# Kernel tuning notes

Hardware: AMD Instinct MI355X
Metric: run time of the kernel (lower is better)

## Reference

```python
import jax, jax.numpy as jnp
import numpy as np

D = 1024
DFF = 4096  # SwiGLU hidden = 4*d_model
EPS = 1e-6

def rmsnorm(x, w):
    return x * jax.lax.rsqrt(jnp.mean(x * x, axis=-1, keepdims=True) + EPS) * w

def mingru_scan(gates, cands):
    # h_t = g_t * h_{t-1} + (1 - g_t) * c_t, h_0 = 0 -> linear recurrence,
    # solved with an associative scan over pairs (a, b): h = a*h_prev + b.
    a = gates
    b = (1.0 - gates) * cands
    def combine(e1, e2):
        a1, b1 = e1
        a2, b2 = e2
        return (a1 * a2, a2 * b1 + b2)
    _, h = jax.lax.associative_scan(combine, (a, b), axis=1)
    return h

def setup_inputs() -> dict:
    key = jax.random.key(0)
    ks = jax.random.split(key, 10)
    xavier = lambda k, fan_in, fan_out: jax.random.uniform(
        k, (fan_in, fan_out), jnp.float32,
        -np.sqrt(6.0 / (fan_in + fan_out)), np.sqrt(6.0 / (fan_in + fan_out)))
    return {
        "x": jax.random.normal(ks[0], (4, 4096, D), jnp.float32),
        "Wg": xavier(ks[1], D, D),
        "bg": jnp.ones((D,), jnp.float32),   # gate bias init = 1.0
        "Wc": xavier(ks[2], D, D),
        "bc": jnp.zeros((D,), jnp.float32),
        "n1_w": jnp.ones((D,), jnp.float32),
        "n2_w": jnp.ones((D,), jnp.float32),
        "W1": xavier(ks[3], D, DFF),   # SwiGLU gate proj
        "W3": xavier(ks[4], D, DFF),   # SwiGLU up proj
        "W2": xavier(ks[5], DFF, D),   # SwiGLU down proj
    }

def reference(x, Wg, bg, Wc, bc, n1_w, n2_w, W1, W3, W2):
    # --- MinGRU sub-block (pre-norm, residual) ---
    h_in = rmsnorm(x, n1_w)
    gates = jax.nn.sigmoid(jnp.einsum('bld,de->ble', h_in, Wg) + bg)
    cands = jnp.tanh(jnp.einsum('bld,de->ble', h_in, Wc) + bc)
    x = x + mingru_scan(gates, cands)
    # --- SwiGLU FFN sub-block (pre-norm, residual) ---
    f_in = rmsnorm(x, n2_w)
    ff = jnp.einsum('blf,fd->bld',
                    jax.nn.silu(jnp.einsum('bld,df->blf', f_in, W1))
                    * jnp.einsum('bld,df->blf', f_in, W3), W2)
    return x + ff
```

## Files before the change

kernel.cpp:

```cpp
#include <hip/hip_runtime.h>
#include <hip/hip_bf16.h>
#include <math.h>

typedef __bf16 bf16_t;
typedef bf16_t bf16x8 __attribute__((ext_vector_type(8)));
typedef bf16_t bf16x4 __attribute__((ext_vector_type(4)));
typedef bf16_t bf16x2 __attribute__((ext_vector_type(2)));
typedef float f32x4 __attribute__((ext_vector_type(4)));

#define D_MODEL 1024
#define SEQ     4096
#define BATCH   4
#define NTOK    16384
#define DFF     4096
#define CLEN    64
#define NCHUNK  64
#define NCH     4096

__device__ __forceinline__ void gload16(const bf16_t* g, bf16_t* l) {
    __builtin_amdgcn_global_load_lds(
        (const __attribute__((address_space(1))) void*)g,
        (__attribute__((address_space(3))) void*)l, 16, 0, 0);
}

__global__ void transpose_to_bf16(const float* __restrict__ W,
                                  bf16_t* __restrict__ Wt, int R, int C) {
    __shared__ float tile[32][33];
    const int c0 = blockIdx.x * 32, r0 = blockIdx.y * 32;
    const int tx = threadIdx.x, ty = threadIdx.y;
#pragma unroll
    for (int j = 0; j < 32; j += 8)
        tile[ty + j][tx] = W[(size_t)(r0 + ty + j) * C + c0 + tx];
    __syncthreads();
#pragma unroll
    for (int j = 0; j < 32; j += 8)
        Wt[(size_t)(c0 + ty + j) * R + r0 + tx] = (bf16_t)tile[tx][ty + j];
}

__global__ void rmsnorm_kernel(const float* __restrict__ x,
                               const float* __restrict__ w,
                               bf16_t* __restrict__ out) {
    const int row = blockIdx.x;
    const int tid = threadIdx.x;
    const float4 v = ((const float4*)(x + (size_t)row * D_MODEL))[tid];
    float ss = v.x * v.x + v.y * v.y + v.z * v.z + v.w * v.w;
#pragma unroll
    for (int o = 1; o < 64; o <<= 1) ss += __shfl_xor(ss, o);
    __shared__ float red[4];
    if ((tid & 63) == 0) red[tid >> 6] = ss;
    __syncthreads();
    const float tot = red[0] + red[1] + red[2] + red[3];
    const float scale = rsqrtf(tot * (1.0f / D_MODEL) + 1e-6f);
    const float4 wv = ((const float4*)w)[tid];
    bf16x4 o4;
    o4[0] = (bf16_t)(v.x * scale * wv.x);
    o4[1] = (bf16_t)(v.y * scale * wv.y);
    o4[2] = (bf16_t)(v.z * scale * wv.z);
    o4[3] = (bf16_t)(v.w * scale * wv.w);
    ((bf16x4*)(out + (size_t)row * D_MODEL))[tid] = o4;
}

template <int MODE>
__global__ __launch_bounds__(256, 2)
void gemm_dual(const bf16_t* __restrict__ A, const bf16_t* __restrict__ B1t,
               const bf16_t* __restrict__ B2t, const float* __restrict__ bias1,
               const float* __restrict__ bias2, bf16x2* __restrict__ GC,
               bf16_t* __restrict__ Ot, int N, int K) {
    __shared__ bf16_t As[128 * 32];
    __shared__ bf16_t B1s[128 * 32];
    __shared__ bf16_t B2s[128 * 32];
    const int tid = threadIdx.x;
    const int lane = tid & 63;
    const int wave = tid >> 6;
    const int bn = blockIdx.x, bm = blockIdx.y;

    const int stR = wave * 16 + (lane >> 2);
    const int stC = (lane & 3) * 8;
    const bf16_t* Ag  = A   + (size_t)(bm * 128 + stR) * K + stC;
    const bf16_t* B1g = B1t + (size_t)(bn * 128 + stR) * K + stC;
    const bf16_t* B2g = B2t + (size_t)(bn * 128 + stR) * K + stC;
    bf16_t* Al0  = &As [(wave * 16) * 32];
    bf16_t* Al1  = &As [(64 + wave * 16) * 32];
    bf16_t* B1l0 = &B1s[(wave * 16) * 32];
    bf16_t* B1l1 = &B1s[(64 + wave * 16) * 32];
    bf16_t* B2l0 = &B2s[(wave * 16) * 32];
    bf16_t* B2l1 = &B2s[(64 + wave * 16) * 32];
    const size_t row64 = (size_t)64 * K;

    const int wr = wave >> 1, wc = wave & 1;
    const int lr = lane & 15, lk = lane >> 4;

    f32x4 acc1[4][4] = {};
    f32x4 acc2[4][4] = {};
    for (int k0 = 0; k0 < K; k0 += 32) {
        __syncthreads();
        gload16(Ag  + k0,         Al0);
        gload16(Ag  + k0 + row64, Al1);
        gload16(B1g + k0,         B1l0);
        gload16(B1g + k0 + row64, B1l1);
        gload16(B2g + k0,         B2l0);
        gload16(B2g + k0 + row64, B2l1);
        __syncthreads();
        bf16x8 af[4], b1f[4], b2f[4];
#pragma unroll
        for (int m = 0; m < 4; ++m)
            af[m] = *(const bf16x8*)&As[(wr * 64 + m * 16 + lr) * 32 + lk * 8];
#pragma unroll
        for (int n = 0; n < 4; ++n) {
            b1f[n] = *(const bf16x8*)&B1s[(wc * 64 + n * 16 + lr) * 32 + lk * 8];
            b2f[n] = *(const bf16x8*)&B2s[(wc * 64 + n * 16 + lr) * 32 + lk * 8];
        }
#pragma unroll
        for (int m = 0; m < 4; ++m)
#pragma unroll
            for (int n = 0; n < 4; ++n) {
                acc1[m][n] = __builtin_amdgcn_mfma_f32_16x16x32_bf16(
                    af[m], b1f[n], acc1[m][n], 0, 0, 0);
                acc2[m][n] = __builtin_amdgcn_mfma_f32_16x16x32_bf16(
                    af[m], b2f[n], acc2[m][n], 0, 0, 0);
            }
    }
    const int rowBase = bm * 128 + wr * 64;
    const int colBase = bn * 128 + wc * 64;
#pragma unroll
    for (int n = 0; n < 4; ++n) {
        const int col = colBase + n * 16 + lr;
        float b1v = 0.f, b2v = 0.f;
        if (MODE == 0) { b1v = bias1[col]; b2v = bias2[col]; }
#pragma unroll
        for (int m = 0; m < 4; ++m) {
#pragma unroll
            for (int j = 0; j < 4; ++j) {
                const int row = rowBase + m * 16 + lk * 4 + j;
                const size_t idx = (size_t)row * N + col;
                if (MODE == 0) {
                    const float gv = 1.0f / (1.0f + __expf(-(acc1[m][n][j] + b1v)));
                    const float cv = tanhf(acc2[m][n][j] + b2v);
                    bf16x2 pk;
                    pk[0] = (bf16_t)gv;
                    pk[1] = (bf16_t)cv;
                    GC[idx] = pk;
                } else {
                    const float a = acc1[m][n][j];
                    const float s = a / (1.0f + __expf(-a));
                    Ot[idx] = (bf16_t)(s * acc2[m][n][j]);
                }
            }
        }
    }
}

__global__ __launch_bounds__(256, 2)
void gemm_res(const bf16_t* __restrict__ A, const bf16_t* __restrict__ Bt,
              float* O, int N, int K) {
    __shared__ bf16_t As[128 * 32];
    __shared__ bf16_t Bs[128 * 32];
    const int tid = threadIdx.x;
    const int lane = tid & 63;
    const int wave = tid >> 6;
    const int bn = blockIdx.x, bm = blockIdx.y;

    const int stR = wave * 16 + (lane >> 2);
    const int stC = (lane & 3) * 8;
    const bf16_t* Ag = A  + (size_t)(bm * 128 + stR) * K + stC;
    const bf16_t* Bg = Bt + (size_t)(bn * 128 + stR) * K + stC;
    bf16_t* Al0 = &As[(wave * 16) * 32];
    bf16_t* Al1 = &As[(64 + wave * 16) * 32];
    bf16_t* Bl0 = &Bs[(wave * 16) * 32];
    bf16_t* Bl1 = &Bs[(64 + wave * 16) * 32];
    const size_t row64 = (size_t)64 * K;

    const int wr = wave >> 1, wc = wave & 1;
    const int lr = lane & 15, lk = lane >> 4;

    f32x4 acc[4][4] = {};
    for (int k0 = 0; k0 < K; k0 += 32) {
        __syncthreads();
        gload16(Ag + k0,         Al0);
        gload16(Ag + k0 + row64, Al1);
        gload16(Bg + k0,         Bl0);
        gload16(Bg + k0 + row64, Bl1);
        __syncthreads();
        bf16x8 af[4], bf[4];
#pragma unroll
        for (int m = 0; m < 4; ++m)
            af[m] = *(const bf16x8*)&As[(wr * 64 + m * 16 + lr) * 32 + lk * 8];
#pragma unroll
        for (int n = 0; n < 4; ++n)
            bf[n] = *(const bf16x8*)&Bs[(wc * 64 + n * 16 + lr) * 32 + lk * 8];
#pragma unroll
        for (int m = 0; m < 4; ++m)
#pragma unroll
            for (int n = 0; n < 4; ++n)
                acc[m][n] = __builtin_amdgcn_mfma_f32_16x16x32_bf16(
                    af[m], bf[n], acc[m][n], 0, 0, 0);
    }
    const int rowBase = bm * 128 + wr * 64;
    const int colBase = bn * 128 + wc * 64;
#pragma unroll
    for (int n = 0; n < 4; ++n) {
        const int col = colBase + n * 16 + lr;
#pragma unroll
        for (int m = 0; m < 4; ++m) {
#pragma unroll
            for (int j = 0; j < 4; ++j) {
                const int row = rowBase + m * 16 + lk * 4 + j;
                const size_t idx = (size_t)row * N + col;
                O[idx] += acc[m][n][j];
            }
        }
    }
}

__global__ void scan_phase1(const bf16x2* __restrict__ gc,
                            float* __restrict__ cA, float* __restrict__ cB) {
    const int d = blockIdx.x * 256 + threadIdx.x;
    const int b = blockIdx.y;
    const int cidx = blockIdx.z;
    const int ch = b * D_MODEL + d;
    const size_t base = ((size_t)b * SEQ + (size_t)cidx * CLEN) * D_MODEL + d;
    float A = 1.0f, Bv = 0.0f;
#pragma unroll 8
    for (int t = 0; t < CLEN; ++t) {
        const bf16x2 v = gc[base + (size_t)t * D_MODEL];
        const float gv = (float)v[0], cv = (float)v[1];
        Bv = gv * Bv + (1.0f - gv) * cv;
        A *= gv;
    }
    cA[cidx * NCH + ch] = A;
    cB[cidx * NCH + ch] = Bv;
}

__global__ void scan_phase2(const float* __restrict__ cA,
                            const float* __restrict__ cB,
                            float* __restrict__ hstart) {
    const int ch = blockIdx.x * 256 + threadIdx.x;
    float h = 0.0f;
#pragma unroll 8
    for (int cdx = 0; cdx < NCHUNK; ++cdx) {
        hstart[cdx * NCH + ch] = h;
        h = cA[cdx * NCH + ch] * h + cB[cdx * NCH + ch];
    }
}

__global__ void scan_phase3(const bf16x2* __restrict__ gc,
                            const float* __restrict__ hstart,
                            const float* __restrict__ x,
                            float* __restrict__ x1) {
    const int d = blockIdx.x * 256 + threadIdx.x;
    const int b = blockIdx.y;
    const int cidx = blockIdx.z;
    const int ch = b * D_MODEL + d;
    const size_t base = ((size_t)b * SEQ + (size_t)cidx * CLEN) * D_MODEL + d;
    float h = hstart[cidx * NCH + ch];
#pragma unroll 8
    for (int t = 0; t < CLEN; ++t) {
        const size_t off = base + (size_t)t * D_MODEL;
        const bf16x2 v = gc[off];
        const float gv = (float)v[0], cv = (float)v[1];
        h = gv * h + (1.0f - gv) * cv;
        x1[off] = x[off] + h;
    }
}

extern "C" void kernel_launch(void* const* d_in, const int* in_sizes, int n_in,
                              void* d_out, int out_size, void* d_ws,
                              size_t ws_size, hipStream_t stream) {
    const float* x   = (const float*)d_in[0];
    const float* Wg  = (const float*)d_in[1];
    const float* bg  = (const float*)d_in[2];
    const float* Wc  = (const float*)d_in[3];
    const float* bc  = (const float*)d_in[4];
    const float* n1w = (const float*)d_in[5];
    const float* n2w = (const float*)d_in[6];
    const float* W1  = (const float*)d_in[7];
    const float* W3  = (const float*)d_in[8];
    const float* W2  = (const float*)d_in[9];
    float* out = (float*)d_out;

    char* p = (char*)d_ws;
    bf16_t* tbuf  = (bf16_t*)p;
    bf16_t* h_in  = (bf16_t*)p;  p += (size_t)NTOK * D_MODEL * 2;
    bf16x2* gcbuf = (bf16x2*)p;  p += (size_t)NTOK * D_MODEL * 4;
    p += (size_t)32 << 20;
    bf16_t* f_in  = (bf16_t*)p;  p += (size_t)NTOK * D_MODEL * 2;
    bf16_t* Wg_t  = (bf16_t*)p;  p += (size_t)D_MODEL * D_MODEL * 2;
    bf16_t* Wc_t  = (bf16_t*)p;  p += (size_t)D_MODEL * D_MODEL * 2;
    bf16_t* W1_t  = (bf16_t*)p;  p += (size_t)DFF * D_MODEL * 2;
    bf16_t* W3_t  = (bf16_t*)p;  p += (size_t)DFF * D_MODEL * 2;
    bf16_t* W2_t  = (bf16_t*)p;  p += (size_t)D_MODEL * DFF * 2;
    float* cA     = (float*)p;   p += (size_t)NCHUNK * NCH * 4;
    float* cB     = (float*)p;   p += (size_t)NCHUNK * NCH * 4;
    float* hstart = (float*)p;   p += (size_t)NCHUNK * NCH * 4;

    const dim3 tb(32, 8);
    transpose_to_bf16<<<dim3(1024 / 32, 1024 / 32), tb, 0, stream>>>(Wg, Wg_t, 1024, 1024);
    transpose_to_bf16<<<dim3(1024 / 32, 1024 / 32), tb, 0, stream>>>(Wc, Wc_t, 1024, 1024);
    transpose_to_bf16<<<dim3(4096 / 32, 1024 / 32), tb, 0, stream>>>(W1, W1_t, 1024, 4096);
    transpose_to_bf16<<<dim3(4096 / 32, 1024 / 32), tb, 0, stream>>>(W3, W3_t, 1024, 4096);
    transpose_to_bf16<<<dim3(1024 / 32, 4096 / 32), tb, 0, stream>>>(W2, W2_t, 4096, 1024);

    rmsnorm_kernel<<<NTOK, 256, 0, stream>>>(x, n1w, h_in);

    gemm_dual<0><<<dim3(D_MODEL / 128, NTOK / 128), 256, 0, stream>>>(
        h_in, Wg_t, Wc_t, bg, bc, gcbuf, nullptr, D_MODEL, D_MODEL);

    scan_phase1<<<dim3(D_MODEL / 256, BATCH, NCHUNK), 256, 0, stream>>>(gcbuf, cA, cB);
    scan_phase2<<<NCH / 256, 256, 0, stream>>>(cA, cB, hstart);
    scan_phase3<<<dim3(D_MODEL / 256, BATCH, NCHUNK), 256, 0, stream>>>(gcbuf, hstart, x, out);

    rmsnorm_kernel<<<NTOK, 256, 0, stream>>>(out, n2w, f_in);

    gemm_dual<1><<<dim3(DFF / 128, NTOK / 128), 256, 0, stream>>>(
        f_in, W1_t, W3_t, nullptr, nullptr, nullptr, tbuf, DFF, D_MODEL);

    gemm_res<<<dim3(D_MODEL / 128, NTOK / 128), 256, 0, stream>>>(tbuf, W2_t, out, D_MODEL, DFF);
}
```

Before: 847.9 us.

## Replace GEMMs with 8-wave double-buffered 256-row tiles, swizzled LDS and ping-pong schedule

Replaces the three GEMM kernels with one templated 512-thread kernel. It uses 256-row tiles, a K-step of 64 and double-buffered LDS staging of the next tile during compute. LDS rows are XOR-swizzled, which targets bank conflicts. Work-group ids are remapped in groups of 8 for cache locality, and barriers plus setprio stagger the MFMA and load phases. The aim is to hide global-load latency and raise MFMA utilisation, at the cost of much larger LDS use (128KB), high register pressure and reduced occupancy.

```diff
diff --git a/kernel.cpp b/kernel.cpp
--- a/kernel.cpp
+++ b/kernel.cpp
@@ -60,153 +60,194 @@
     ((bf16x4*)(out + (size_t)row * D_MODEL))[tid] = o4;
 }
 
+#define MFMA16(a, b, c) __builtin_amdgcn_mfma_f32_16x16x32_bf16((a), (b), (c), 0, 0, 0)
+
 template <int MODE>
-__global__ __launch_bounds__(256, 2)
-void gemm_dual(const bf16_t* __restrict__ A, const bf16_t* __restrict__ B1t,
-               const bf16_t* __restrict__ B2t, const float* __restrict__ bias1,
-               const float* __restrict__ bias2, bf16x2* __restrict__ GC,
-               bf16_t* __restrict__ Ot, int N, int K) {
-    __shared__ bf16_t As[128 * 32];
-    __shared__ bf16_t B1s[128 * 32];
-    __shared__ bf16_t B2s[128 * 32];
+__global__ __launch_bounds__(512, 2)
+void gemm8p(const bf16_t* __restrict__ A, const bf16_t* __restrict__ B1t,
+            const bf16_t* __restrict__ B2t, const float* __restrict__ bias1,
+            const float* __restrict__ bias2, bf16x2* __restrict__ GC,
+            bf16_t* __restrict__ Ot, float* __restrict__ O,
+            int N, int K, int lg_nbn) {
+    constexpr bool DUAL = (MODE != 2);
+    constexpr int BN = DUAL ? 128 : 256;
+    constexpr int NFR = DUAL ? 2 : 4;
+    __shared__ bf16_t lds[65536];
+
     const int tid = threadIdx.x;
     const int lane = tid & 63;
     const int wave = tid >> 6;
-    const int bn = blockIdx.x, bm = blockIdx.y;
-
-    const int stR = wave * 16 + (lane >> 2);
-    const int stC = (lane & 3) * 8;
-    const bf16_t* Ag  = A   + (size_t)(bm * 128 + stR) * K + stC;
-    const bf16_t* B1g = B1t + (size_t)(bn * 128 + stR) * K + stC;
-    const bf16_t* B2g = B2t + (size_t)(bn * 128 + stR) * K + stC;
-    bf16_t* Al0  = &As [(wave * 16) * 32];
-    bf16_t* Al1  = &As [(64 + wave * 16) * 32];
-    bf16_t* B1l0 = &B1s[(wave * 16) * 32];
-    bf16_t* B1l1 = &B1s[(64 + wave * 16) * 32];
-    bf16_t* B2l0 = &B2s[(wave * 16) * 32];
-    bf16_t* B2l1 = &B2s[(64 + wave * 16) * 32];
-    const size_t row64 = (size_t)64 * K;
-
-    const int wr = wave >> 1, wc = wave & 1;
-    const int lr = lane & 15, lk = lane >> 4;
-
-    f32x4 acc1[4][4] = {};
-    f32x4 acc2[4][4] = {};
-    for (int k0 = 0; k0 < K; k0 += 32) {
-        __syncthreads();
-        gload16(Ag  + k0,         Al0);
-        gload16(Ag  + k0 + row64, Al1);
-        gload16(B1g + k0,         B1l0);
-        gload16(B1g + k0 + row64, B1l1);
-        gload16(B2g + k0,         B2l0);
-        gload16(B2g + k0 + row64, B2l1);
-        __syncthreads();
-        bf16x8 af[4], b1f[4], b2f[4];
+    const int wr = wave >> 2, wc = wave & 3;
+    const int lr16 = lane & 15, lk = lane >> 4;
+
+    const int nwg = gridDim.x;
+    const int wg = blockIdx.x;
+    const int swg = (wg & 7) * (nwg >> 3) + (wg >> 3);
+    const int bn = swg & ((1 << lg_nbn) - 1);
+    const int bm = swg >> lg_nbn;
+    const int nt = K >> 6;
+
+    const int lr8 = lane >> 3;
+    const int cge = ((lane & 7) ^ lr8) << 3;
+    const bf16_t* Ag  = A   + (size_t)(bm * 256 + wave * 8 + lr8) * K + cge;
+    const bf16_t* B1g = B1t + (size_t)(bn * BN  + wave * 8 + lr8) * K + cge;
+    const bf16_t* B2g = DUAL ? (B2t + (size_t)(bn * BN + wave * 8 + lr8) * K + cge)
+                             : (const bf16_t*)nullptr;
+
+    f32x4 acc1[8][NFR] = {};
+    f32x4 acc2[DUAL ? 8 : 1][NFR] = {};
+
+    auto stageA = [&](int u) {
+        bf16_t* dst = &lds[(u & 1) * 32768 + wave * 512];
+        const bf16_t* src = Ag + ((size_t)u << 6);
+        gload16(src,                     dst);
+        gload16(src + ((size_t)64  * K), dst + 4096);
+        gload16(src + ((size_t)128 * K), dst + 8192);
+        gload16(src + ((size_t)192 * K), dst + 12288);
+    };
+    auto stageB = [&](int u) {
+        bf16_t* dst = &lds[(u & 1) * 32768 + 16384 + wave * 512];
+        const bf16_t* src = B1g + ((size_t)u << 6);
+        gload16(src,                    dst);
+        gload16(src + ((size_t)64 * K), dst + 4096);
+        if constexpr (DUAL) {
+            bf16_t* dst2 = &lds[(u & 1) * 32768 + 24576 + wave * 512];
+            const bf16_t* src2 = B2g + ((size_t)u << 6);
+            gload16(src2,                    dst2);
+            gload16(src2 + ((size_t)64 * K), dst2 + 4096);
+        } else {
+            gload16(src + ((size_t)128 * K), dst + 8192);
+            gload16(src + ((size_t)192 * K), dst + 12288);
+        }
+    };
+    auto rdA = [&](int p, int m, int ks) {
+        const int row = wr * 128 + m * 16 + lr16;
+        const int c = ks * 4 + lk;
+        return *(const bf16x8*)&lds[p * 32768 + row * 64 + (((c ^ row) & 7) << 3)];
+    };
+    auto rdB = [&](int p, int mat, int n, int ks) {
+        const int row = wc * (BN / 4) + n * 16 + lr16;
+        const int c = ks * 4 + lk;
+        return *(const bf16x8*)&lds[p * 32768 + 16384 + mat * 8192 + row * 64 +
+                                    (((c ^ row) & 7) << 3)];
+    };
+
+    stageA(0);
+    stageB(0);
+    asm volatile("s_waitcnt vmcnt(0)" ::: "memory");
+    __builtin_amdgcn_s_barrier();
+
+    for (int t = 0; t < nt; ++t) {
+        const int p = t & 1;
+        const bool pre = (t + 1 < nt);
+        bf16x8 bF[DUAL ? 2 : 1][NFR];
+        bf16x8 aF[4];
+
+#pragma unroll
+        for (int n = 0; n < NFR; ++n) {
+            bF[0][n] = rdB(p, 0, n, 0);
+            if constexpr (DUAL) bF[1][n] = rdB(p, 1, n, 0);
+        }
+#pragma unroll
+        for (int m = 0; m < 4; ++m) aF[m] = rdA(p, m, 0);
+        if (pre) stageA(t + 1);
+        __builtin_amdgcn_s_barrier();
+        asm volatile("s_waitcnt lgkmcnt(0)" ::: "memory");
+        __builtin_amdgcn_sched_barrier(0);
+        __builtin_amdgcn_s_setprio(1);
 #pragma unroll
         for (int m = 0; m < 4; ++m)
-            af[m] = *(const bf16x8*)&As[(wr * 64 + m * 16 + lr) * 32 + lk * 8];
-#pragma unroll
-        for (int n = 0; n < 4; ++n) {
-            b1f[n] = *(const bf16x8*)&B1s[(wc * 64 + n * 16 + lr) * 32 + lk * 8];
-            b2f[n] = *(const bf16x8*)&B2s[(wc * 64 + n * 16 + lr) * 32 + lk * 8];
+#pragma unroll
+            for (int n = 0; n < NFR; ++n) {
+                acc1[m][n] = MFMA16(aF[m], bF[0][n], acc1[m][n]);
+                if constexpr (DUAL) acc2[m][n] = MFMA16(aF[m], bF[1][n], acc2[m][n]);
+            }
+        __builtin_amdgcn_s_setprio(0);
+        __builtin_amdgcn_s_barrier();
+
+#pragma unroll
+        for (int m = 0; m < 4; ++m) aF[m] = rdA(p, 4 + m, 0);
+        if (pre) stageB(t + 1);
+        __builtin_amdgcn_s_barrier();
+        asm volatile("s_waitcnt lgkmcnt(0)" ::: "memory");
+        __builtin_amdgcn_sched_barrier(0);
+        __builtin_amdgcn_s_setprio(1);
+#pragma unroll
+        for (int m = 0; m < 4; ++m)
+#pragma unroll
+            for (int n = 0; n < NFR; ++n) {
+                acc1[4 + m][n] = MFMA16(aF[m], bF[0][n], acc1[4 + m][n]);
+                if constexpr (DUAL) acc2[4 + m][n] = MFMA16(aF[m], bF[1][n], acc2[4 + m][n]);
+            }
+        __builtin_amdgcn_s_setprio(0);
+        __builtin_amdgcn_s_barrier();
+
+#pragma unroll
+        for (int n = 0; n < NFR; ++n) {
+            bF[0][n] = rdB(p, 0, n, 1);
+            if constexpr (DUAL) bF[1][n] = rdB(p, 1, n, 1);
         }
 #pragma unroll
+        for (int m = 0; m < 4; ++m) aF[m] = rdA(p, m, 1);
+        __builtin_amdgcn_s_barrier();
+        asm volatile("s_waitcnt lgkmcnt(0)" ::: "memory");
+        __builtin_amdgcn_sched_barrier(0);
+        __builtin_amdgcn_s_setprio(1);
+#pragma unroll
         for (int m = 0; m < 4; ++m)
 #pragma unroll
-            for (int n = 0; n < 4; ++n) {
-                acc1[m][n] = __builtin_amdgcn_mfma_f32_16x16x32_bf16(
-                    af[m], b1f[n], acc1[m][n], 0, 0, 0);
-                acc2[m][n] = __builtin_amdgcn_mfma_f32_16x16x32_bf16(
-                    af[m], b2f[n], acc2[m][n], 0, 0, 0);
-            }
-    }
-    const int rowBase = bm * 128 + wr * 64;
-    const int colBase = bn * 128 + wc * 64;
-#pragma unroll
-    for (int n = 0; n < 4; ++n) {
-        const int col = colBase + n * 16 + lr;
+            for (int n = 0; n < NFR; ++n) {
+                acc1[m][n] = MFMA16(aF[m], bF[0][n], acc1[m][n]);
+                if constexpr (DUAL) acc2[m][n] = MFMA16(aF[m], bF[1][n], acc2[m][n]);
+            }
+        __builtin_amdgcn_s_setprio(0);
+        __builtin_amdgcn_s_barrier();
+
+#pragma unroll
+        for (int m = 0; m < 4; ++m) aF[m] = rdA(p, 4 + m, 1);
+        __builtin_amdgcn_s_barrier();
+        asm volatile("s_waitcnt lgkmcnt(0)" ::: "memory");
+        __builtin_amdgcn_sched_barrier(0);
+        __builtin_amdgcn_s_setprio(1);
+#pragma unroll
+        for (int m = 0; m < 4; ++m)
+#pragma unroll
+            for (int n = 0; n < NFR; ++n) {
+                acc1[4 + m][n] = MFMA16(aF[m], bF[0][n], acc1[4 + m][n]);
+                if constexpr (DUAL) acc2[4 + m][n] = MFMA16(aF[m], bF[1][n], acc2[4 + m][n]);
+            }
+        __builtin_amdgcn_s_setprio(0);
+        asm volatile("s_waitcnt vmcnt(0)" ::: "memory");
+        __builtin_amdgcn_s_barrier();
+    }
+
+    const int rowBase = bm * 256 + wr * 128;
+    const int colBase = bn * BN + wc * (BN / 4);
+#pragma unroll
+    for (int n = 0; n < NFR; ++n) {
+        const int col = colBase + n * 16 + lr16;
         float b1v = 0.f, b2v = 0.f;
-        if (MODE == 0) { b1v = bias1[col]; b2v = bias2[col]; }
-#pragma unroll
-        for (int m = 0; m < 4; ++m) {
+        if constexpr (MODE == 0) { b1v = bias1[col]; b2v = bias2[col]; }
+#pragma unroll
+        for (int m = 0; m < 8; ++m) {
 #pragma unroll
             for (int j = 0; j < 4; ++j) {
                 const int row = rowBase + m * 16 + lk * 4 + j;
                 const size_t idx = (size_t)row * N + col;
-                if (MODE == 0) {
+                if constexpr (MODE == 0) {
                     const float gv = 1.0f / (1.0f + __expf(-(acc1[m][n][j] + b1v)));
                     const float cv = tanhf(acc2[m][n][j] + b2v);
                     bf16x2 pk;
                     pk[0] = (bf16_t)gv;
                     pk[1] = (bf16_t)cv;
                     GC[idx] = pk;
-                } else {
+                } else if constexpr (MODE == 1) {
                     const float a = acc1[m][n][j];
                     const float s = a / (1.0f + __expf(-a));
                     Ot[idx] = (bf16_t)(s * acc2[m][n][j]);
+                } else {
+                    O[idx] += acc1[m][n][j];
                 }
-            }
-        }
-    }
-}
-
-__global__ __launch_bounds__(256, 2)
-void gemm_res(const bf16_t* __restrict__ A, const bf16_t* __restrict__ Bt,
-              float* O, int N, int K) {
-    __shared__ bf16_t As[128 * 32];
-    __shared__ bf16_t Bs[128 * 32];
-    const int tid = threadIdx.x;
-    const int lane = tid & 63;
-    const int wave = tid >> 6;
-    const int bn = blockIdx.x, bm = blockIdx.y;
-
-    const int stR = wave * 16 + (lane >> 2);
-    const int stC = (lane & 3) * 8;
-    const bf16_t* Ag = A  + (size_t)(bm * 128 + stR) * K + stC;
-    const bf16_t* Bg = Bt + (size_t)(bn * 128 + stR) * K + stC;
-    bf16_t* Al0 = &As[(wave * 16) * 32];
-    bf16_t* Al1 = &As[(64 + wave * 16) * 32];
-    bf16_t* Bl0 = &Bs[(wave * 16) * 32];
-    bf16_t* Bl1 = &Bs[(64 + wave * 16) * 32];
-    const size_t row64 = (size_t)64 * K;
-
-    const int wr = wave >> 1, wc = wave & 1;
-    const int lr = lane & 15, lk = lane >> 4;
-
-    f32x4 acc[4][4] = {};
-    for (int k0 = 0; k0 < K; k0 += 32) {
-        __syncthreads();
-        gload16(Ag + k0,         Al0);
-        gload16(Ag + k0 + row64, Al1);
-        gload16(Bg + k0,         Bl0);
-        gload16(Bg + k0 + row64, Bl1);
-        __syncthreads();
-        bf16x8 af[4], bf[4];
-#pragma unroll
-        for (int m = 0; m < 4; ++m)
-            af[m] = *(const bf16x8*)&As[(wr * 64 + m * 16 + lr) * 32 + lk * 8];
-#pragma unroll
-        for (int n = 0; n < 4; ++n)
-            bf[n] = *(const bf16x8*)&Bs[(wc * 64 + n * 16 + lr) * 32 + lk * 8];
-#pragma unroll
-        for (int m = 0; m < 4; ++m)
-#pragma unroll
-            for (int n = 0; n < 4; ++n)
-                acc[m][n] = __builtin_amdgcn_mfma_f32_16x16x32_bf16(
-                    af[m], bf[n], acc[m][n], 0, 0, 0);
-    }
-    const int rowBase = bm * 128 + wr * 64;
-    const int colBase = bn * 128 + wc * 64;
-#pragma unroll
-    for (int n = 0; n < 4; ++n) {
-        const int col = colBase + n * 16 + lr;
-#pragma unroll
-        for (int m = 0; m < 4; ++m) {
-#pragma unroll
-            for (int j = 0; j < 4; ++j) {
-                const int row = rowBase + m * 16 + lk * 4 + j;
-                const size_t idx = (size_t)row * N + col;
-                O[idx] += acc[m][n][j];
             }
         }
     }
@@ -302,8 +343,8 @@
 
     rmsnorm_kernel<<<NTOK, 256, 0, stream>>>(x, n1w, h_in);
 
-    gemm_dual<0><<<dim3(D_MODEL / 128, NTOK / 128), 256, 0, stream>>>(
-        h_in, Wg_t, Wc_t, bg, bc, gcbuf, nullptr, D_MODEL, D_MODEL);
+    gemm8p<0><<<512, 512, 0, stream>>>(h_in, Wg_t, Wc_t, bg, bc, gcbuf,
+                                       nullptr, nullptr, D_MODEL, D_MODEL, 3);
 
     scan_phase1<<<dim3(D_MODEL / 256, BATCH, NCHUNK), 256, 0, stream>>>(gcbuf, cA, cB);
     scan_phase2<<<NCH / 256, 256, 0, stream>>>(cA, cB, hstart);
@@ -311,8 +352,9 @@
 
     rmsnorm_kernel<<<NTOK, 256, 0, stream>>>(out, n2w, f_in);
 
-    gemm_dual<1><<<dim3(DFF / 128, NTOK / 128), 256, 0, stream>>>(
-        f_in, W1_t, W3_t, nullptr, nullptr, nullptr, tbuf, DFF, D_MODEL);
-
-    gemm_res<<<dim3(D_MODEL / 128, NTOK / 128), 256, 0, stream>>>(tbuf, W2_t, out, D_MODEL, DFF);
-}
+    gemm8p<1><<<2048, 512, 0, stream>>>(f_in, W1_t, W3_t, nullptr, nullptr,
+                                        nullptr, tbuf, nullptr, DFF, D_MODEL, 5);
+
+    gemm8p<2><<<256, 512, 0, stream>>>(tbuf, W2_t, nullptr, nullptr, nullptr,
+                                       nullptr, nullptr, out, D_MODEL, DFF, 2);
+}
```

Result: faster. 765.1 us (-9.8%).
